# Performance work log

Hardware: AMD Instinct MI355X
Metric: run time of the kernel (lower is better)

Reference implementation:

```python
import jax, jax.numpy as jnp
import numpy as np

N_NODES = 50000
N_EDGES = 800000
D_IN = 64
D_HID = 64
N_GRAPHS = 64


def setup_inputs() -> dict:
    key = jax.random.key(0)
    ks = jax.random.split(key, 10)
    x = jax.random.normal(ks[0], (N_NODES, D_IN), dtype=jnp.float32)
    edge_index = jax.random.randint(ks[1], (2, N_EDGES), 0, N_NODES, dtype=jnp.int64)
    batch = jnp.sort(jax.random.randint(ks[2], (N_NODES,), 0, N_GRAPHS, dtype=jnp.int64))
    s1 = 1.0 / np.sqrt(D_IN)
    s2 = 1.0 / np.sqrt(D_HID)
    W1 = jax.random.uniform(ks[3], (D_IN, D_HID), jnp.float32, -s1, s1)
    b1 = jnp.zeros((D_HID,), jnp.float32)
    W2 = jax.random.uniform(ks[4], (D_HID, D_HID), jnp.float32, -s2, s2)
    b2 = jnp.zeros((D_HID,), jnp.float32)
    W3 = jax.random.uniform(ks[5], (D_HID, D_HID), jnp.float32, -s2, s2)
    b3 = jnpp = jnp.zeros((D_HID,), jnp.float32)
    return {"x": x, "edge_index": edge_index, "batch": batch,
            "W1": W1, "b1": b1, "W2": W2, "b2": b2, "W3": W3, "b3": b3}


def _gcn_norm(edge_index, num_nodes):
    # add self-loops, then symmetric normalization deg^-1/2 A_hat deg^-1/2
    loop = jnp.arange(num_nodes, dtype=edge_index.dtype)
    row = jnp.concatenate([edge_index[0], loop])  # source
    col = jnp.concatenate([edge_index[1], loop])  # target (aggregation index)
    deg = jax.ops.segment_sum(jnp.ones_like(col, dtype=jnp.float32), col,
                              num_segments=num_nodes)
    dinv = jnp.where(deg > 0, jax.lax.rsqrt(deg), 0.0)
    norm = dinv[row] * dinv[col]  # [E+N]
    return row, col, norm


def _gcn_conv(x, row, col, norm, W, b, num_nodes):
    h = x @ W                                   # [N, D] small GEMM
    msg = h[row] * norm[:, None]                # edge-wise gather + scale
    out = jax.ops.segment_sum(msg, col, num_segments=num_nodes)  # scatter-add
    return out + b


def reference(x, edge_index, batch, W1, b1, W2, b2, W3, b3):
    n = x.shape[0]
    row, col, norm = _gcn_norm(edge_index, n)
    h = jax.nn.relu(_gcn_conv(x, row, col, norm, W1, b1, n))
    h = jax.nn.relu(_gcn_conv(h, row, col, norm, W2, b2, n))
    h = jax.nn.relu(_gcn_conv(h, row, col, norm, W3, b3, n))
    # global_mean_pool over graphs
    sums = jax.ops.segment_sum(h, batch, num_segments=N_GRAPHS)
    cnt = jax.ops.segment_sum(jnp.ones((n,), jnp.float32), batch,
                              num_segments=N_GRAPHS)
    return sums / jnp.maximum(cnt, 1.0)[:, None]
```

## Files before the change

kernel.cpp:

```cpp
#include <hip/hip_runtime.h>

#define N_NODES   50000
#define N_EDGES   800000
#define DF        64
#define N_GRAPHS  64
#define NPAD      50176

#define ABLK 200
#define AEDG (N_EDGES/ABLK)
#define RSH  9
#define NREG 98
#define RPAD 128
#define CAP  12288

__global__ __launch_bounds__(256)
void k_hist(const int* __restrict__ col, int* __restrict__ H,
            float* __restrict__ pool) {
    __shared__ int h[RPAD];
    const int t = threadIdx.x, b = blockIdx.x;
    if (b == 0)
        for (int i = t; i < N_GRAPHS * DF; i += 256) pool[i] = 0.f;
    if (t < RPAD) h[t] = 0;
    __syncthreads();
    const int e0 = b * AEDG;
    for (int i = t; i < AEDG; i += 256)
        atomicAdd(&h[col[e0 + i] >> RSH], 1);
    __syncthreads();
    if (t < RPAD) H[t * ABLK + b] = h[t];
}

__global__ __launch_bounds__(256)
void k_scanH(const int* __restrict__ H, int* __restrict__ O,
             int* __restrict__ T) {
    __shared__ int s[256];
    const int t = threadIdx.x, r = blockIdx.x;
    int v = (t < ABLK) ? H[r * ABLK + t] : 0;
    s[t] = v; __syncthreads();
    #pragma unroll
    for (int off = 1; off < 256; off <<= 1) {
        int x = (t >= off) ? s[t - off] : 0;
        __syncthreads();
        s[t] += x;
        __syncthreads();
    }
    if (t < ABLK) O[r * ABLK + t] = s[t] - v;
    if (t == 255) T[r] = s[255];
}

__global__ __launch_bounds__(256)
void k_bin(const int* __restrict__ row, const int* __restrict__ col,
           const int* __restrict__ O, const int* __restrict__ T,
           unsigned* __restrict__ staging) {
    __shared__ int cur[RPAD];
    __shared__ int rs[RPAD];
    const int t = threadIdx.x, b = blockIdx.x;
    int v = 0;
    if (t < RPAD) { v = T[t]; rs[t] = v; }
    __syncthreads();
    #pragma unroll
    for (int off = 1; off < RPAD; off <<= 1) {
        int x = 0;
        if (t < RPAD && t >= off) x = rs[t - off];
        __syncthreads();
        if (t < RPAD) rs[t] += x;
        __syncthreads();
    }
    if (t < RPAD) cur[t] = O[t * ABLK + b] + (rs[t] - v);
    __syncthreads();
    const int e0 = b * AEDG;
    for (int i = t; i < AEDG; i += 256) {
        int c = col[e0 + i];
        int rr = row[e0 + i];
        int slot = atomicAdd(&cur[c >> RSH], 1);
        staging[slot] = ((unsigned)c << 16) | (unsigned)rr;
    }
}

__global__ __launch_bounds__(512)
void k_csr(const unsigned* __restrict__ staging, const int* __restrict__ T,
           int* __restrict__ offs, float* __restrict__ dinv,
           int* __restrict__ esrc) {
    __shared__ int hist[512];
    __shared__ int cur[512];
    __shared__ int img[CAP];
    __shared__ int rs[RPAD];
    __shared__ int sh_s0, sh_s1;
    const int t = threadIdx.x, r = blockIdx.x;
    int v = 0;
    if (t < RPAD) { v = T[t]; rs[t] = v; }
    __syncthreads();
    #pragma unroll
    for (int off = 1; off < RPAD; off <<= 1) {
        int x = 0;
        if (t < RPAD && t >= off) x = rs[t - off];
        __syncthreads();
        if (t < RPAD) rs[t] += x;
        __syncthreads();
    }
    if (t == r) { sh_s0 = rs[t] - v; sh_s1 = rs[t]; }
    hist[t] = 0;
    __syncthreads();
    const int s0 = sh_s0, s1 = sh_s1;
    for (int i = s0 + t; i < s1; i += 512) {
        int ln = (int)(staging[i] >> 16) - (r << RSH);
        atomicAdd(&hist[ln], 1);
    }
    __syncthreads();
    int myc = hist[t];
    #pragma unroll
    for (int off = 1; off < 512; off <<= 1) {
        int x = (t >= off) ? hist[t - off] : 0;
        __syncthreads();
        hist[t] += x;
        __syncthreads();
    }
    int excl = hist[t] - myc;
    int n = (r << RSH) + t;
    offs[n] = s0 + excl;
    if (n < N_NODES) dinv[n] = rsqrtf((float)(myc + 1));
    cur[t] = excl;
    __syncthreads();
    for (int i = s0 + t; i < s1; i += 512) {
        unsigned p = staging[i];
        int ln = (int)(p >> 16) - (r << RSH);
        int rr = (int)(p & 0xFFFFu);
        int slot = atomicAdd(&cur[ln], 1);
        if (slot < CAP) img[slot] = rr;
        else           esrc[s0 + slot] = rr;
    }
    __syncthreads();
    int cnt = s1 - s0; if (cnt > CAP) cnt = CAP;
    for (int j = t; j < cnt; j += 512) esrc[s0 + j] = img[j];
}

#define FB_ROWS 64
#define NPW 8
#define LDX 68

__global__ __launch_bounds__(512, 4)
void k_fused(const int* __restrict__ offs, const int* __restrict__ esrc,
             const float* __restrict__ dinv, const float* __restrict__ h,
             const float* __restrict__ W, const float* __restrict__ bias,
             float* __restrict__ out, const int* __restrict__ batch,
             float* __restrict__ pool) {
    __shared__ float XsT[DF][LDX];
    __shared__ float Ws[DF][DF];
    __shared__ float plocal[4 * DF];
    __shared__ int   sh_batch[FB_ROWS];

    const int t = threadIdx.x;
    const int row0 = blockIdx.x * FB_ROWS;

    for (int idx = t * 4; idx < DF * DF; idx += 512 * 4) {
        float4 w = *(const float4*)&W[idx];
        Ws[idx >> 6][(idx & 63) + 0] = w.x;
        Ws[idx >> 6][(idx & 63) + 1] = w.y;
        Ws[idx >> 6][(idx & 63) + 2] = w.z;
        Ws[idx >> 6][(idx & 63) + 3] = w.w;
    }
    if (pool) {
        if (t < 4 * DF) plocal[t] = 0.f;
        if (t < FB_ROWS) {
            int n = row0 + t;
            sh_batch[t] = batch[n < N_NODES ? n : N_NODES - 1];
        }
    }

    const int wv = t >> 6;
    const int l  = t & 63;
    const int g  = l >> 4;
    const int q  = l & 15;
    for (int ii = 0; ii < NPW; ++ii) {
        const int r = wv * NPW + ii;
        const int n = row0 + r;
        if (n >= N_NODES) break;

        const float dc = dinv[n];
        float ax = 0.f, ay = 0.f, az = 0.f, aw = 0.f;

        if (g == 0) {
            float4 xv = *(const float4*)&h[n * DF + q * 4];
            ax = xv.x * dc; ay = xv.y * dc; az = xv.z * dc; aw = xv.w * dc;
        }

        const int s1 = offs[n + 1];
        int s = offs[n];
        for (; s + 16 <= s1; s += 16) {
            int r0 = esrc[s + g];
            int r1 = esrc[s + 4 + g];
            int r2 = esrc[s + 8 + g];
            int r3 = esrc[s + 12 + g];
            float w0 = dinv[r0], w1 = dinv[r1], w2 = dinv[r2], w3 = dinv[r3];
            float4 v0 = *(const float4*)&h[r0 * DF + q * 4];
            float4 v1 = *(const float4*)&h[r1 * DF + q * 4];
            float4 v2 = *(const float4*)&h[r2 * DF + q * 4];
            float4 v3 = *(const float4*)&h[r3 * DF + q * 4];
            ax += v0.x * w0; ay += v0.y * w0; az += v0.z * w0; aw += v0.w * w0;
            ax += v1.x * w1; ay += v1.y * w1; az += v1.z * w1; aw += v1.w * w1;
            ax += v2.x * w2; ay += v2.y * w2; az += v2.z * w2; aw += v2.w * w2;
            ax += v3.x * w3; ay += v3.y * w3; az += v3.z * w3; aw += v3.w * w3;
        }
        for (; s + 8 <= s1; s += 8) {
            int r0 = esrc[s + g];
            int r1 = esrc[s + 4 + g];
            float w0 = dinv[r0], w1 = dinv[r1];
            float4 v0 = *(const float4*)&h[r0 * DF + q * 4];
            float4 v1 = *(const float4*)&h[r1 * DF + q * 4];
            ax += v0.x * w0; ay += v0.y * w0; az += v0.z * w0; aw += v0.w * w0;
            ax += v1.x * w1; ay += v1.y * w1; az += v1.z * w1; aw += v1.w * w1;
        }
        for (; s < s1; s += 4) {
            int idx = s + g;
            bool valid = idx < s1;
            int rr = valid ? esrc[idx] : n;
            float w = valid ? dinv[rr] : 0.f;
            float4 v = *(const float4*)&h[rr * DF + q * 4];
            ax += v.x * w; ay += v.y * w; az += v.z * w; aw += v.w * w;
        }

        ax += __shfl_xor(ax, 16); ay += __shfl_xor(ay, 16);
        az += __shfl_xor(az, 16); aw += __shfl_xor(aw, 16);
        ax += __shfl_xor(ax, 32); ay += __shfl_xor(ay, 32);
        az += __shfl_xor(az, 32); aw += __shfl_xor(aw, 32);

        if (l < 16) {
            XsT[q * 4 + 0][r] = ax * dc;
            XsT[q * 4 + 1][r] = ay * dc;
            XsT[q * 4 + 2][r] = az * dc;
            XsT[q * 4 + 3][r] = aw * dc;
        }
    }
    __syncthreads();

    const int i = (t & 15) * 4;
    const int j = (t >> 4) * 2;
    float acc[4][2] = {};
    #pragma unroll 8
    for (int k = 0; k < DF; ++k) {
        float4 xv = *(const float4*)&XsT[k][i];
        float2 wvv = *(const float2*)&Ws[k][j];
        acc[0][0] += xv.x * wvv.x; acc[0][1] += xv.x * wvv.y;
        acc[1][0] += xv.y * wvv.x; acc[1][1] += xv.y * wvv.y;
        acc[2][0] += xv.z * wvv.x; acc[2][1] += xv.z * wvv.y;
        acc[3][0] += xv.w * wvv.x; acc[3][1] += xv.w * wvv.y;
    }
    const float bx = bias[j], by = bias[j + 1];

    if (!pool) {
        #pragma unroll
        for (int u = 0; u < 4; ++u) {
            int gr = row0 + i + u;
            if (gr < N_NODES) {
                float ox = acc[u][0] + bx;
                float oy = acc[u][1] + by;
                ox = ox > 0.f ? ox : 0.f;
                oy = oy > 0.f ? oy : 0.f;
                *(float2*)&out[gr * DF + j] = make_float2(ox, oy);
            }
        }
    } else {
        const int g0 = sh_batch[0];
        const int span = sh_batch[FB_ROWS - 1] - g0 + 1;
        if (span <= 4) {
            #pragma unroll
            for (int u = 0; u < 4; ++u) {
                int gr = row0 + i + u;
                if (gr < N_NODES) {
                    float ox = acc[u][0] + bx;
                    float oy = acc[u][1] + by;
                    ox = ox > 0.f ? ox : 0.f;
                    oy = oy > 0.f ? oy : 0.f;
                    int gl = sh_batch[i + u] - g0;
                    atomicAdd(&plocal[gl * DF + j],     ox);
                    atomicAdd(&plocal[gl * DF + j + 1], oy);
                }
            }
            __syncthreads();
            for (int idx = t; idx < span * DF; idx += 512)
                atomicAdd(&pool[g0 * DF + idx], plocal[idx]);
        } else {
            #pragma unroll
            for (int u = 0; u < 4; ++u) {
                int gr = row0 + i + u;
                if (gr < N_NODES) {
                    float ox = acc[u][0] + bx;
                    float oy = acc[u][1] + by;
                    ox = ox > 0.f ? ox : 0.f;
                    oy = oy > 0.f ? oy : 0.f;
                    int gg = sh_batch[i + u];
                    atomicAdd(&pool[gg * DF + j],     ox);
                    atomicAdd(&pool[gg * DF + j + 1], oy);
                }
            }
        }
    }
}

__device__ __forceinline__ int lb(const int* a, int n, int key) {
    int lo = 0, hi = n;
    while (lo < hi) { int m = (lo + hi) >> 1; if (a[m] < key) lo = m + 1; else hi = m; }
    return lo;
}

__global__ void k_div(const float* __restrict__ pool, const int* __restrict__ batch,
                      float* __restrict__ out) {
    int idx = blockIdx.x * blockDim.x + threadIdx.x;
    if (idx < N_GRAPHS * DF) {
        int g = idx >> 6;
        int c = lb(batch, N_NODES, g + 1) - lb(batch, N_NODES, g);
        out[idx] = pool[idx] / fmaxf((float)c, 1.0f);
    }
}


extern "C" void kernel_launch(void* const* d_in, const int* in_sizes, int n_in,
                              void* d_out, int out_size, void* d_ws, size_t ws_size,
                              hipStream_t stream) {
    const float* x     = (const float*)d_in[0];
    const int*   ei    = (const int*)d_in[1];
    const int*   batch = (const int*)d_in[2];
    const float* W1    = (const float*)d_in[3];
    const float* b1    = (const float*)d_in[4];
    const float* W2    = (const float*)d_in[5];
    const float* b2    = (const float*)d_in[6];
    const float* W3    = (const float*)d_in[7];
    const float* b3    = (const float*)d_in[8];
    float* out = (float*)d_out;

    const int* row = ei;
    const int* col = ei + N_EDGES;

    char* wsb = (char*)d_ws;
    float*    pool    = (float*)wsb;
    int*      H       = (int*)(pool + N_GRAPHS * DF);
    int*      O       = H + RPAD * ABLK;
    int*      T       = O + RPAD * ABLK;
    int*      offs    = T + RPAD;
    int*      esrc    = offs + NPAD;
    unsigned* staging = (unsigned*)(esrc + N_EDGES);
    float*    dinv    = (float*)(staging + N_EDGES);
    float*    bufA    = dinv + NPAD;
    float*    bufB    = bufA + N_NODES * DF;

    const int nblk_F = (N_NODES + FB_ROWS - 1) / FB_ROWS;

    k_hist<<<ABLK, 256, 0, stream>>>(col, H, pool);
    k_scanH<<<RPAD, 256, 0, stream>>>(H, O, T);
    k_bin<<<ABLK, 256, 0, stream>>>(row, col, O, T, staging);
    k_csr<<<NREG, 512, 0, stream>>>(staging, T, offs, dinv, esrc);

    k_fused<<<nblk_F, 512, 0, stream>>>(offs, esrc, dinv, x,    W1, b1, bufA,
                                        nullptr, nullptr);
    k_fused<<<nblk_F, 512, 0, stream>>>(offs, esrc, dinv, bufA, W2, b2, bufB,
                                        nullptr, nullptr);
    k_fused<<<nblk_F, 512, 0, stream>>>(offs, esrc, dinv, bufB, W3, b3, nullptr,
                                        batch, pool);

    k_div<<<(N_GRAPHS * DF + 255) / 256, 256, 0, stream>>>(pool, batch, out);
}
```

Measured before the change: 262.5 us.

## Balance edge work across waves with packed edges and shared-memory atomic accumulation

The CSR build now packs each edge's local destination index into the upper 16 bits next to its source id. The fused aggregation kernel splits the block's contiguous edge range evenly across its 8 waves, instead of assigning 8 fixed rows per wave. Each wave accumulates runs of edges that share a destination in registers, then flushes them with LDS float atomics into a row-major accumulator tile seeded with the self-loop term. This is meant to fix load imbalance from varying node degrees, at the cost of LDS atomics, run-boundary flushes and a non-deterministic summation order. The GEMM reads from a padded row-major tile instead of the transposed one.

```diff
diff --git a/kernel.cpp b/kernel.cpp
--- a/kernel.cpp
+++ b/kernel.cpp
@@ -79,10 +79,10 @@
 __global__ __launch_bounds__(512)
 void k_csr(const unsigned* __restrict__ staging, const int* __restrict__ T,
            int* __restrict__ offs, float* __restrict__ dinv,
-           int* __restrict__ esrc) {
+           unsigned* __restrict__ epack) {
     __shared__ int hist[512];
     __shared__ int cur[512];
-    __shared__ int img[CAP];
+    __shared__ unsigned img[CAP];
     __shared__ int rs[RPAD];
     __shared__ int sh_s0, sh_s1;
     const int t = threadIdx.x, r = blockIdx.x;
@@ -123,30 +123,32 @@
     for (int i = s0 + t; i < s1; i += 512) {
         unsigned p = staging[i];
         int ln = (int)(p >> 16) - (r << RSH);
-        int rr = (int)(p & 0xFFFFu);
+        unsigned rr = p & 0xFFFFu;
+        unsigned pk = rr | ((unsigned)ln << 16);
         int slot = atomicAdd(&cur[ln], 1);
-        if (slot < CAP) img[slot] = rr;
-        else           esrc[s0 + slot] = rr;
+        if (slot < CAP) img[slot] = pk;
+        else           epack[s0 + slot] = pk;
     }
     __syncthreads();
     int cnt = s1 - s0; if (cnt > CAP) cnt = CAP;
-    for (int j = t; j < cnt; j += 512) esrc[s0 + j] = img[j];
+    for (int j = t; j < cnt; j += 512) epack[s0 + j] = img[j];
 }
 
 #define FB_ROWS 64
-#define NPW 8
-#define LDX 68
+#define LDA 65
 
 __global__ __launch_bounds__(512, 4)
-void k_fused(const int* __restrict__ offs, const int* __restrict__ esrc,
+void k_fused(const int* __restrict__ offs, const unsigned* __restrict__ epack,
              const float* __restrict__ dinv, const float* __restrict__ h,
              const float* __restrict__ W, const float* __restrict__ bias,
              float* __restrict__ out, const int* __restrict__ batch,
              float* __restrict__ pool) {
-    __shared__ float XsT[DF][LDX];
+    __shared__ float Xacc[FB_ROWS][LDA];
     __shared__ float Ws[DF][DF];
+    __shared__ float sh_dinv[FB_ROWS];
     __shared__ float plocal[4 * DF];
     __shared__ int   sh_batch[FB_ROWS];
+    __shared__ int   sh_e0, sh_e1;
 
     const int t = threadIdx.x;
     const int row0 = blockIdx.x * FB_ROWS;
@@ -158,6 +160,12 @@
         Ws[idx >> 6][(idx & 63) + 2] = w.z;
         Ws[idx >> 6][(idx & 63) + 3] = w.w;
     }
+    if (t == 0) sh_e0 = offs[row0];
+    if (t == 1) sh_e1 = offs[row0 + FB_ROWS];
+    if (t < FB_ROWS) {
+        int n = row0 + t;
+        sh_dinv[t] = (n < N_NODES) ? dinv[n] : 0.f;
+    }
     if (pool) {
         if (t < 4 * DF) plocal[t] = 0.f;
         if (t < FB_ROWS) {
@@ -170,66 +178,71 @@
     const int l  = t & 63;
     const int g  = l >> 4;
     const int q  = l & 15;
-    for (int ii = 0; ii < NPW; ++ii) {
-        const int r = wv * NPW + ii;
-        const int n = row0 + r;
-        if (n >= N_NODES) break;
-
-        const float dc = dinv[n];
-        float ax = 0.f, ay = 0.f, az = 0.f, aw = 0.f;
-
-        if (g == 0) {
-            float4 xv = *(const float4*)&h[n * DF + q * 4];
-            ax = xv.x * dc; ay = xv.y * dc; az = xv.z * dc; aw = xv.w * dc;
+
+    for (int ii = 0; ii < 8; ++ii) {
+        int r = wv * 8 + ii;
+        int n = row0 + r;
+        if (l < 16) {
+            float4 o = make_float4(0.f, 0.f, 0.f, 0.f);
+            if (n < N_NODES) {
+                float dc = dinv[n];
+                float s  = dc * dc;
+                float4 xv = *(const float4*)&h[n * DF + q * 4];
+                o.x = s * xv.x; o.y = s * xv.y; o.z = s * xv.z; o.w = s * xv.w;
+            }
+            Xacc[r][q * 4 + 0] = o.x;
+            Xacc[r][q * 4 + 1] = o.y;
+            Xacc[r][q * 4 + 2] = o.z;
+            Xacc[r][q * 4 + 3] = o.w;
         }
-
-        const int s1 = offs[n + 1];
-        int s = offs[n];
-        for (; s + 16 <= s1; s += 16) {
-            int r0 = esrc[s + g];
-            int r1 = esrc[s + 4 + g];
-            int r2 = esrc[s + 8 + g];
-            int r3 = esrc[s + 12 + g];
-            float w0 = dinv[r0], w1 = dinv[r1], w2 = dinv[r2], w3 = dinv[r3];
-            float4 v0 = *(const float4*)&h[r0 * DF + q * 4];
-            float4 v1 = *(const float4*)&h[r1 * DF + q * 4];
-            float4 v2 = *(const float4*)&h[r2 * DF + q * 4];
-            float4 v3 = *(const float4*)&h[r3 * DF + q * 4];
-            ax += v0.x * w0; ay += v0.y * w0; az += v0.z * w0; aw += v0.w * w0;
-            ax += v1.x * w1; ay += v1.y * w1; az += v1.z * w1; aw += v1.w * w1;
-            ax += v2.x * w2; ay += v2.y * w2; az += v2.z * w2; aw += v2.w * w2;
-            ax += v3.x * w3; ay += v3.y * w3; az += v3.z * w3; aw += v3.w * w3;
-        }
-        for (; s + 8 <= s1; s += 8) {
-            int r0 = esrc[s + g];
-            int r1 = esrc[s + 4 + g];
-            float w0 = dinv[r0], w1 = dinv[r1];
-            float4 v0 = *(const float4*)&h[r0 * DF + q * 4];
-            float4 v1 = *(const float4*)&h[r1 * DF + q * 4];
-            ax += v0.x * w0; ay += v0.y * w0; az += v0.z * w0; aw += v0.w * w0;
-            ax += v1.x * w1; ay += v1.y * w1; az += v1.z * w1; aw += v1.w * w1;
-        }
-        for (; s < s1; s += 4) {
-            int idx = s + g;
-            bool valid = idx < s1;
-            int rr = valid ? esrc[idx] : n;
-            float w = valid ? dinv[rr] : 0.f;
-            float4 v = *(const float4*)&h[rr * DF + q * 4];
-            ax += v.x * w; ay += v.y * w; az += v.z * w; aw += v.w * w;
-        }
-
-        ax += __shfl_xor(ax, 16); ay += __shfl_xor(ay, 16);
-        az += __shfl_xor(az, 16); aw += __shfl_xor(aw, 16);
-        ax += __shfl_xor(ax, 32); ay += __shfl_xor(ay, 32);
-        az += __shfl_xor(az, 32); aw += __shfl_xor(aw, 32);
-
-        if (l < 16) {
-            XsT[q * 4 + 0][r] = ax * dc;
-            XsT[q * 4 + 1][r] = ay * dc;
-            XsT[q * 4 + 2][r] = az * dc;
-            XsT[q * 4 + 3][r] = aw * dc;
-        }
-    }
+    }
+    __syncthreads();
+
+    const int e0 = sh_e0, e1 = sh_e1;
+    const int cnt = e1 - e0;
+    const int chunk = (cnt + 7) >> 3;
+    const int wsrt = e0 + wv * chunk;
+    int we = wsrt + chunk; if (we > e1) we = e1;
+
+    const int base_ln = row0 & ((1 << RSH) - 1);
+    int cur = -1;
+    float ax = 0.f, ay = 0.f, az = 0.f, aw = 0.f;
+
+#define FLUSH() do { float sd = sh_dinv[cur];                       \
+        atomicAdd(&Xacc[cur][(q << 2) + 0], ax * sd);               \
+        atomicAdd(&Xacc[cur][(q << 2) + 1], ay * sd);               \
+        atomicAdd(&Xacc[cur][(q << 2) + 2], az * sd);               \
+        atomicAdd(&Xacc[cur][(q << 2) + 3], aw * sd);               \
+        ax = ay = az = aw = 0.f; } while (0)
+
+    int e = wsrt + g;
+    for (; e + 4 < we; e += 8) {
+        unsigned p0 = epack[e];
+        unsigned p1 = epack[e + 4];
+        int r0 = (int)(p0 & 0xFFFFu);
+        int r1 = (int)(p1 & 0xFFFFu);
+        int c0 = (int)(p0 >> 16) - base_ln;
+        int c1 = (int)(p1 >> 16) - base_ln;
+        float w0 = dinv[r0];
+        float w1 = dinv[r1];
+        float4 v0 = *(const float4*)&h[(r0 << 6) + (q << 2)];
+        float4 v1 = *(const float4*)&h[(r1 << 6) + (q << 2)];
+        if (c0 != cur) { if (cur >= 0) FLUSH(); cur = c0; }
+        ax += v0.x * w0; ay += v0.y * w0; az += v0.z * w0; aw += v0.w * w0;
+        if (c1 != cur) { FLUSH(); cur = c1; }
+        ax += v1.x * w1; ay += v1.y * w1; az += v1.z * w1; aw += v1.w * w1;
+    }
+    for (; e < we; e += 4) {
+        unsigned p0 = epack[e];
+        int r0 = (int)(p0 & 0xFFFFu);
+        int c0 = (int)(p0 >> 16) - base_ln;
+        float w0 = dinv[r0];
+        float4 v0 = *(const float4*)&h[(r0 << 6) + (q << 2)];
+        if (c0 != cur) { if (cur >= 0) FLUSH(); cur = c0; }
+        ax += v0.x * w0; ay += v0.y * w0; az += v0.z * w0; aw += v0.w * w0;
+    }
+    if (cur >= 0) FLUSH();
+#undef FLUSH
     __syncthreads();
 
     const int i = (t & 15) * 4;
@@ -237,12 +250,15 @@
     float acc[4][2] = {};
     #pragma unroll 8
     for (int k = 0; k < DF; ++k) {
-        float4 xv = *(const float4*)&XsT[k][i];
+        float x0 = Xacc[i + 0][k];
+        float x1 = Xacc[i + 1][k];
+        float x2 = Xacc[i + 2][k];
+        float x3 = Xacc[i + 3][k];
         float2 wvv = *(const float2*)&Ws[k][j];
-        acc[0][0] += xv.x * wvv.x; acc[0][1] += xv.x * wvv.y;
-        acc[1][0] += xv.y * wvv.x; acc[1][1] += xv.y * wvv.y;
-        acc[2][0] += xv.z * wvv.x; acc[2][1] += xv.z * wvv.y;
-        acc[3][0] += xv.w * wvv.x; acc[3][1] += xv.w * wvv.y;
+        acc[0][0] += x0 * wvv.x; acc[0][1] += x0 * wvv.y;
+        acc[1][0] += x1 * wvv.x; acc[1][1] += x1 * wvv.y;
+        acc[2][0] += x2 * wvv.x; acc[2][1] += x2 * wvv.y;
+        acc[3][0] += x3 * wvv.x; acc[3][1] += x3 * wvv.y;
     }
     const float bx = bias[j], by = bias[j + 1];
 
@@ -336,8 +352,8 @@
     int*      O       = H + RPAD * ABLK;
     int*      T       = O + RPAD * ABLK;
     int*      offs    = T + RPAD;
-    int*      esrc    = offs + NPAD;
-    unsigned* staging = (unsigned*)(esrc + N_EDGES);
+    unsigned* epack   = (unsigned*)(offs + NPAD);
+    unsigned* staging = epack + N_EDGES;
     float*    dinv    = (float*)(staging + N_EDGES);
     float*    bufA    = dinv + NPAD;
     float*    bufB    = bufA + N_NODES * DF;
@@ -347,13 +363,13 @@
     k_hist<<<ABLK, 256, 0, stream>>>(col, H, pool);
     k_scanH<<<RPAD, 256, 0, stream>>>(H, O, T);
     k_bin<<<ABLK, 256, 0, stream>>>(row, col, O, T, staging);
-    k_csr<<<NREG, 512, 0, stream>>>(staging, T, offs, dinv, esrc);
-
-    k_fused<<<nblk_F, 512, 0, stream>>>(offs, esrc, dinv, x,    W1, b1, bufA,
+    k_csr<<<NREG, 512, 0, stream>>>(staging, T, offs, dinv, epack);
+
+    k_fused<<<nblk_F, 512, 0, stream>>>(offs, epack, dinv, x,    W1, b1, bufA,
                                         nullptr, nullptr);
-    k_fused<<<nblk_F, 512, 0, stream>>>(offs, esrc, dinv, bufA, W2, b2, bufB,
+    k_fused<<<nblk_F, 512, 0, stream>>>(offs, epack, dinv, bufA, W2, b2, bufB,
                                         nullptr, nullptr);
-    k_fused<<<nblk_F, 512, 0, stream>>>(offs, esrc, dinv, bufB, W3, b3, nullptr,
+    k_fused<<<nblk_F, 512, 0, stream>>>(offs, epack, dinv, bufB, W3, b3, nullptr,
                                         batch, pool);
 
     k_div<<<(N_GRAPHS * DF + 255) / 256, 256, 0, stream>>>(pool, batch, out);
```

After: 484.9 us. 84.7% more time.
